# Kernel tuning notes

Hardware: AMD Instinct MI355X
Metric: run time of the kernel (lower is better)

The kernel has to match this reference:

```python
import jax, jax.numpy as jnp
import numpy as np

D_L = 64
HIDDEN = 64
CUBE = (D_L + 1) ** 3  # 274625


def setup_inputs() -> dict:
    key = jax.random.key(0)
    ks = jax.random.split(key, 9)
    B = 512
    l = jax.random.normal(ks[0], (B, D_L), dtype=jnp.float32)
    a = jax.random.normal(ks[1], (B, D_L), dtype=jnp.float32)
    v = jax.random.normal(ks[2], (B, D_L), dtype=jnp.float32)
    # Linear params (xavier-ish scale)
    W1 = jax.random.normal(ks[3], (CUBE, HIDDEN), dtype=jnp.float32) * (1.0 / np.sqrt(CUBE))
    b1 = jnp.zeros((HIDDEN,), dtype=jnp.float32)
    W2 = jax.random.normal(ks[4], (HIDDEN, HIDDEN), dtype=jnp.float32) * (1.0 / np.sqrt(HIDDEN))
    b2 = jnp.zeros((HIDDEN,), dtype=jnp.float32)
    W3 = jax.random.normal(ks[5], (HIDDEN, D_L), dtype=jnp.float32) * (1.0 / np.sqrt(HIDDEN))
    b3 = jnp.zeros((D_L,), dtype=jnp.float32)
    return {"l": l, "a": a, "v": v, "W1": W1, "b1": b1, "W2": W2, "b2": b2, "W3": W3, "b3": b3}


def reference(l, a, v, W1, b1, W2, b2, W3, b3):
    B = a.shape[0]
    ones = jnp.ones((B, 1), dtype=a.dtype)
    a_h = jnp.concatenate([ones, a], axis=1)  # [B, d+1]
    v_h = jnp.concatenate([ones, v], axis=1)
    t_h = jnp.concatenate([ones, l], axis=1)
    # fusion[b, i, j, k] = a_h[b,i] * v_h[b,j] * t_h[b,k]; flattened row-major (i,j,k)
    fusion = jnp.einsum('bi,bj,bk->bijk', a_h, v_h, t_h).reshape(B, -1)  # [B, (d+1)^3]
    h = jnp.tanh(fusion @ W1 + b1)
    h = jnp.tanh(h @ W2 + b2)
    out = jnp.tanh(h @ W3 + b3)
    return out
```

## Files before the change

### kernel.cpp

```cpp
#include <hip/hip_runtime.h>
#include <hip/hip_fp16.h>


typedef _Float16 f16;
typedef f16 f16x8 __attribute__((ext_vector_type(8)));
typedef f16 f16x2 __attribute__((ext_vector_type(2)));
typedef float f32x4 __attribute__((ext_vector_type(4)));

#define WS_AT      0
#define WS_VT      131072
#define WS_A16     262144
#define WS_V16     327680
#define WS_L16     393216
#define WS_PART    458752

__global__ __launch_bounds__(256) void prep_kernel(
    const float* __restrict__ l, const float* __restrict__ a, const float* __restrict__ v,
    float* __restrict__ aT, float* __restrict__ vT,
    f16* __restrict__ a16, f16* __restrict__ v16, f16* __restrict__ l16)
{
  int g = blockIdx.x * 256 + threadIdx.x;
  int which = g >> 15;
  int idx = g & 32767;
  switch (which) {
    case 0: aT[idx] = a[((idx & 511) << 6) + (idx >> 9)]; break;
    case 1: vT[idx] = v[((idx & 511) << 6) + (idx >> 9)]; break;
    case 2: a16[idx] = (f16)a[idx]; break;
    case 3: v16[idx] = (f16)v[idx]; break;
    case 4: l16[idx] = (f16)l[idx]; break;
  }
}

__device__ __forceinline__ void seg_decode(int s, int& ia, int& iv, int& isel,
                                           int& rowbase, int& rowstride) {
  if (s < 4096)      { int i = s >> 6, j = s & 63; ia = i; iv = j; isel = 0;
                       rowbase = (i+1)*4225 + (j+1)*65 + 1; rowstride = 1; }
  else if (s < 4160) { int i = s - 4096; ia = i; iv = -1; isel = 2;
                       rowbase = (i+1)*4225 + 65; rowstride = 65; }
  else if (s < 4224) { int i = s - 4160; ia = i; iv = -1; isel = 0;
                       rowbase = (i+1)*4225 + 1; rowstride = 1; }
  else if (s < 4288) { int j = s - 4224; ia = -1; iv = j; isel = 0;
                       rowbase = (j+1)*65 + 1; rowstride = 1; }
  else if (s == 4288){ ia = -1; iv = -1; isel = 1; rowbase = 4225; rowstride = 4225; }
  else if (s == 4289){ ia = -1; iv = -1; isel = 2; rowbase = 65;   rowstride = 65; }
  else               { ia = -1; iv = -1; isel = 0; rowbase = 1;    rowstride = 1; }
}

__global__ __launch_bounds__(512, 2) void fusion_gemm(
    const float* __restrict__ W1,
    const float* __restrict__ aT, const float* __restrict__ vT,
    const f16* __restrict__ a16, const f16* __restrict__ v16, const f16* __restrict__ l16,
    f16* __restrict__ partials)
{
  __shared__ f16 l_lds[512 * 64];
  __shared__ f16 btile[2][64 * 64];
  __shared__ f16 pl[2][512];

  const int tid  = threadIdx.x;
  const int bid  = blockIdx.x;
  const int lane = tid & 63;
  const int wave = tid >> 6;
  const int l15  = lane & 15;
  const int l4   = lane >> 4;

  #pragma unroll
  for (int it = 0; it < 8; ++it) {
    int idx = (it << 9) + tid;
    int row = idx >> 3, ch = idx & 7;
    f16x8 val = *(const f16x8*)(l16 + (idx << 3));
    *(f16x8*)&l_lds[(row << 6) + ((ch ^ (row & 7)) << 3)] = val;
  }

  const int s0   = bid * 16 + min(bid, 195);
  const int nseg = 16 + (bid < 195 ? 1 : 0);

  f32x4 acc[4][4] = {};

  const int n_st = tid & 63;
  const int g_st = tid >> 6;

  float wv[8]; float spa, spv;

  {
    int ia, iv, isel, rb, rs;
    seg_decode(s0, ia, iv, isel, rb, rs);
    const float* src = W1 + (long)(rb + g_st * 8 * rs) * 64 + n_st;
    #pragma unroll
    for (int r = 0; r < 8; ++r) wv[r] = src[(long)r * rs * 64];
    spa = (ia >= 0) ? aT[(ia << 9) + tid] : 1.0f;
    spv = (iv >= 0) ? vT[(iv << 9) + tid] : 1.0f;
  }

  for (int ss = 0; ss < nseg; ++ss) {
    const int buf = ss & 1;
    {
      f16x8 c;
      #pragma unroll
      for (int r = 0; r < 8; ++r) c[r] = (f16)wv[r];
      *(f16x8*)&btile[buf][(n_st << 6) + ((g_st ^ (n_st & 7)) << 3)] = c;
      pl[buf][tid] = (f16)(spa * spv);
    }
    if (ss + 1 < nseg) {
      int ia, iv, isel, rb, rs;
      seg_decode(s0 + ss + 1, ia, iv, isel, rb, rs);
      const float* src = W1 + (long)(rb + g_st * 8 * rs) * 64 + n_st;
      #pragma unroll
      for (int r = 0; r < 8; ++r) wv[r] = src[(long)r * rs * 64];
      spa = (ia >= 0) ? aT[(ia << 9) + tid] : 1.0f;
      spv = (iv >= 0) ? vT[(iv << 9) + tid] : 1.0f;
    }
    __syncthreads();
    {
      int ia, iv, isel, rb, rs;
      seg_decode(s0 + ss, ia, iv, isel, rb, rs);
      const f16* gptr = (isel == 1) ? a16 : v16;
      #pragma unroll
      for (int ks = 0; ks < 2; ++ks) {
        f16x8 bf[4], af[4];
        #pragma unroll
        for (int nt = 0; nt < 4; ++nt) {
          int n = (nt << 4) + l15;
          bf[nt] = *(const f16x8*)&btile[buf][(n << 6) + ((((ks << 2) + l4) ^ (n & 7)) << 3)];
        }
        #pragma unroll
        for (int mt = 0; mt < 4; ++mt) {
          int b = (wave << 6) + (mt << 4) + l15;
          f16 p = pl[buf][b];
          f16x8 lv;
          if (isel == 0) {
            lv = *(const f16x8*)&l_lds[(b << 6) + ((((ks << 2) + l4) ^ (b & 7)) << 3)];
          } else {
            lv = *(const f16x8*)(gptr + (b << 6) + (ks << 5) + (l4 << 3));
          }
          f16x2 pp = { p, p };
          f16x2* lvp = (f16x2*)&lv;
          f16x2* afp = (f16x2*)&af[mt];
          afp[0] = lvp[0] * pp; afp[1] = lvp[1] * pp;
          afp[2] = lvp[2] * pp; afp[3] = lvp[3] * pp;
        }
        #pragma unroll
        for (int mt = 0; mt < 4; ++mt)
          #pragma unroll
          for (int nt = 0; nt < 4; ++nt)
            acc[mt][nt] = __builtin_amdgcn_mfma_f32_16x16x32_f16(af[mt], bf[nt], acc[mt][nt], 0, 0, 0);
      }
    }
  }

  #pragma unroll
  for (int mt = 0; mt < 4; ++mt)
    #pragma unroll
    for (int nt = 0; nt < 4; ++nt)
      #pragma unroll
      for (int r = 0; r < 4; ++r) {
        int row = (wave << 6) + (mt << 4) + (l4 << 2) + r;
        int col = (nt << 4) + l15;
        partials[(((long)bid << 9) + row) * 64 + col] = (f16)acc[mt][nt][r];
      }
}

__global__ __launch_bounds__(256) void tail_kernel(
    const f16* __restrict__ partials, const float* __restrict__ W1, const float* __restrict__ b1,
    const float* __restrict__ W2, const float* __restrict__ b2,
    const float* __restrict__ W3, const float* __restrict__ b3, float* __restrict__ out)
{
  __shared__ float red[4][64];
  __shared__ float hbuf[64];
  __shared__ float h2buf[64];
  const int row = blockIdx.x;
  const int t = threadIdx.x;
  const int n = t & 63;
  const int q = t >> 6;

  float s_[4] = {0.f, 0.f, 0.f, 0.f};
  for (int i = 0; i < 64; i += 4) {
    #pragma unroll
    for (int u = 0; u < 4; ++u) {
      int p = ((i + u) << 2) + q;
      s_[u] += (float)partials[((((long)p << 9) + row) << 6) + n];
    }
  }
  red[q][n] = s_[0] + s_[1] + s_[2] + s_[3];
  __syncthreads();
  if (t < 64) {
    float h = red[0][n] + red[1][n] + red[2][n] + red[3][n] + b1[n] + W1[n];
    hbuf[n] = tanhf(h);
  }
  __syncthreads();
  if (t < 64) {
    float acc = b2[n];
    #pragma unroll 8
    for (int k = 0; k < 64; ++k) acc += hbuf[k] * W2[(k << 6) + n];
    h2buf[n] = tanhf(acc);
  }
  __syncthreads();
  if (t < 64) {
    float acc = b3[n];
    #pragma unroll 8
    for (int k = 0; k < 64; ++k) acc += h2buf[k] * W3[(k << 6) + n];
    out[(row << 6) + n] = tanhf(acc);
  }
}

extern "C" void kernel_launch(void* const* d_in, const int* in_sizes, int n_in,
                              void* d_out, int out_size, void* d_ws, size_t ws_size,
                              hipStream_t stream) {
  const float* l  = (const float*)d_in[0];
  const float* a  = (const float*)d_in[1];
  const float* v  = (const float*)d_in[2];
  const float* W1 = (const float*)d_in[3];
  const float* b1 = (const float*)d_in[4];
  const float* W2 = (const float*)d_in[5];
  const float* b2 = (const float*)d_in[6];
  const float* W3 = (const float*)d_in[7];
  const float* b3 = (const float*)d_in[8];
  float* out = (float*)d_out;

  char* ws = (char*)d_ws;
  float* aT  = (float*)(ws + WS_AT);
  float* vT  = (float*)(ws + WS_VT);
  f16*   a16 = (f16*)(ws + WS_A16);
  f16*   v16 = (f16*)(ws + WS_V16);
  f16*   l16 = (f16*)(ws + WS_L16);
  f16*   partials = (f16*)(ws + WS_PART);

  hipLaunchKernelGGL(prep_kernel, dim3(640), dim3(256), 0, stream,
                     l, a, v, aT, vT, a16, v16, l16);
  hipLaunchKernelGGL(fusion_gemm, dim3(256), dim3(512), 0, stream,
                     W1, aT, vT, a16, v16, l16, partials);
  hipLaunchKernelGGL(tail_kernel, dim3(512), dim3(256), 0, stream,
                     partials, W1, b1, W2, b2, W3, b3, out);
}
```

Measured before the change: 63.01 us.

## Restructure fusion GEMM to 1024-thread blocks with register-resident l fragments

The fusion GEMM now launches 1024 threads per block, with two half-blocks each staging one W1 segment so two segments are processed per barrier. Blocks take a fixed 18 segments each, and out-of-range segments are zeroed through a new decode sentinel. The l operand moves from a 64KB LDS copy into per-wave registers, and each wave covers 32 rows instead of 64, which cuts LDS use and raises occupancy. The partials layout is transposed to row-major per batch row so the tail kernel can do contiguous vectorized reads; the tradeoff is more threads per block and higher register pressure.

```diff
diff --git a/kernel.cpp b/kernel.cpp
--- a/kernel.cpp
+++ b/kernel.cpp
@@ -43,18 +43,18 @@
                        rowbase = (j+1)*65 + 1; rowstride = 1; }
   else if (s == 4288){ ia = -1; iv = -1; isel = 1; rowbase = 4225; rowstride = 4225; }
   else if (s == 4289){ ia = -1; iv = -1; isel = 2; rowbase = 65;   rowstride = 65; }
-  else               { ia = -1; iv = -1; isel = 0; rowbase = 1;    rowstride = 1; }
-}
-
-__global__ __launch_bounds__(512, 2) void fusion_gemm(
+  else if (s == 4290){ ia = -1; iv = -1; isel = 0; rowbase = 1;    rowstride = 1; }
+  else               { ia = -2; iv = -1; isel = 0; rowbase = 1;    rowstride = 1; }
+}
+
+__global__ __launch_bounds__(1024, 4) void fusion_gemm(
     const float* __restrict__ W1,
     const float* __restrict__ aT, const float* __restrict__ vT,
     const f16* __restrict__ a16, const f16* __restrict__ v16, const f16* __restrict__ l16,
     f16* __restrict__ partials)
 {
-  __shared__ f16 l_lds[512 * 64];
-  __shared__ f16 btile[2][64 * 64];
-  __shared__ f16 pl[2][512];
+  __shared__ f16 btile[4][64 * 64];
+  __shared__ f16 pl[4][512];
 
   const int tid  = threadIdx.x;
   const int bid  = blockIdx.x;
@@ -62,100 +62,106 @@
   const int wave = tid >> 6;
   const int l15  = lane & 15;
   const int l4   = lane >> 4;
-
-  #pragma unroll
-  for (int it = 0; it < 8; ++it) {
-    int idx = (it << 9) + tid;
-    int row = idx >> 3, ch = idx & 7;
-    f16x8 val = *(const f16x8*)(l16 + (idx << 3));
-    *(f16x8*)&l_lds[(row << 6) + ((ch ^ (row & 7)) << 3)] = val;
-  }
-
-  const int s0   = bid * 16 + min(bid, 195);
-  const int nseg = 16 + (bid < 195 ? 1 : 0);
-
-  f32x4 acc[4][4] = {};
-
-  const int n_st = tid & 63;
-  const int g_st = tid >> 6;
-
-  float wv[8]; float spa, spv;
-
-  {
-    int ia, iv, isel, rb, rs;
-    seg_decode(s0, ia, iv, isel, rb, rs);
-    const float* src = W1 + (long)(rb + g_st * 8 * rs) * 64 + n_st;
-    #pragma unroll
-    for (int r = 0; r < 8; ++r) wv[r] = src[(long)r * rs * 64];
-    spa = (ia >= 0) ? aT[(ia << 9) + tid] : 1.0f;
-    spv = (iv >= 0) ? vT[(iv << 9) + tid] : 1.0f;
-  }
-
-  for (int ss = 0; ss < nseg; ++ss) {
-    const int buf = ss & 1;
+  const int h    = tid >> 9;
+  const int t9   = tid & 511;
+  const int n_st = t9 & 63;
+  const int g_st = t9 >> 6;
+
+  f16x8 lfrag[2][2];
+  #pragma unroll
+  for (int mt = 0; mt < 2; ++mt) {
+    int row = (wave << 5) + (mt << 4) + l15;
+    #pragma unroll
+    for (int ks = 0; ks < 2; ++ks)
+      lfrag[mt][ks] = *(const f16x8*)(l16 + (row << 6) + (ks << 5) + (l4 << 3));
+  }
+
+  f32x4 acc[2][4] = {};
+
+  float wv[2][8];
+  float sp[2][2];
+
+#define ISSUE_LOADS(SET, SEG) do {                                              \
+    int ia_, iv_, isel_, rb_, rs_; seg_decode((SEG), ia_, iv_, isel_, rb_, rs_);\
+    const int rs64_ = rs_ << 6;                                                 \
+    const float* src_ = W1 + (size_t)rb_ * 64 + (size_t)(g_st << 3) * rs64_ + n_st; \
+    _Pragma("unroll")                                                           \
+    for (int r_ = 0; r_ < 8; ++r_) wv[SET][r_] = src_[(size_t)r_ * rs64_];      \
+    sp[SET][0] = (ia_ >= 0) ? aT[(ia_ << 9) + t9] : (ia_ == -1 ? 1.0f : 0.0f);  \
+    sp[SET][1] = (iv_ >= 0) ? vT[(iv_ << 9) + t9] : 1.0f;                       \
+  } while (0)
+
+  ISSUE_LOADS(0, bid * 18 + h);
+
+  #pragma unroll
+  for (int pp = 0; pp < 9; ++pp) {
+    const int cur = pp & 1;
+    const int sbw = (cur << 1) + h;
     {
       f16x8 c;
-      #pragma unroll
-      for (int r = 0; r < 8; ++r) c[r] = (f16)wv[r];
-      *(f16x8*)&btile[buf][(n_st << 6) + ((g_st ^ (n_st & 7)) << 3)] = c;
-      pl[buf][tid] = (f16)(spa * spv);
+      if (cur == 0) {
+        #pragma unroll
+        for (int r = 0; r < 8; ++r) c[r] = (f16)wv[0][r];
+      } else {
+        #pragma unroll
+        for (int r = 0; r < 8; ++r) c[r] = (f16)wv[1][r];
+      }
+      *(f16x8*)&btile[sbw][(n_st << 6) + ((g_st ^ (n_st & 7)) << 3)] = c;
+      pl[sbw][t9] = (f16)(sp[cur][0] * sp[cur][1]);
     }
-    if (ss + 1 < nseg) {
-      int ia, iv, isel, rb, rs;
-      seg_decode(s0 + ss + 1, ia, iv, isel, rb, rs);
-      const float* src = W1 + (long)(rb + g_st * 8 * rs) * 64 + n_st;
-      #pragma unroll
-      for (int r = 0; r < 8; ++r) wv[r] = src[(long)r * rs * 64];
-      spa = (ia >= 0) ? aT[(ia << 9) + tid] : 1.0f;
-      spv = (iv >= 0) ? vT[(iv << 9) + tid] : 1.0f;
+    if (pp < 8) {
+      if (cur == 0) ISSUE_LOADS(1, bid * 18 + (pp + 1) * 2 + h);
+      else          ISSUE_LOADS(0, bid * 18 + (pp + 1) * 2 + h);
     }
-    __syncthreads();
-    {
-      int ia, iv, isel, rb, rs;
-      seg_decode(s0 + ss, ia, iv, isel, rb, rs);
-      const f16* gptr = (isel == 1) ? a16 : v16;
+    asm volatile("s_waitcnt lgkmcnt(0)\n\ts_barrier" ::: "memory");
+    __builtin_amdgcn_sched_barrier(0);
+
+    #pragma unroll
+    for (int sidx = 0; sidx < 2; ++sidx) {
+      const int sb = (cur << 1) + sidx;
+      int s = bid * 18 + pp * 2 + sidx;
+      int ia_, iv_, isel, rb_, rs_;
+      seg_decode(s, ia_, iv_, isel, rb_, rs_);
+      const f16* gsrc = (isel == 1) ? a16 : v16;
       #pragma unroll
       for (int ks = 0; ks < 2; ++ks) {
-        f16x8 bf[4], af[4];
+        f16x8 bf[4];
         #pragma unroll
         for (int nt = 0; nt < 4; ++nt) {
           int n = (nt << 4) + l15;
-          bf[nt] = *(const f16x8*)&btile[buf][(n << 6) + ((((ks << 2) + l4) ^ (n & 7)) << 3)];
+          bf[nt] = *(const f16x8*)&btile[sb][(n << 6) + ((((ks << 2) + l4) ^ (n & 7)) << 3)];
         }
         #pragma unroll
-        for (int mt = 0; mt < 4; ++mt) {
-          int b = (wave << 6) + (mt << 4) + l15;
-          f16 p = pl[buf][b];
+        for (int mt = 0; mt < 2; ++mt) {
+          int row = (wave << 5) + (mt << 4) + l15;
+          f16 ps = pl[sb][row];
           f16x8 lv;
-          if (isel == 0) {
-            lv = *(const f16x8*)&l_lds[(b << 6) + ((((ks << 2) + l4) ^ (b & 7)) << 3)];
-          } else {
-            lv = *(const f16x8*)(gptr + (b << 6) + (ks << 5) + (l4 << 3));
-          }
-          f16x2 pp = { p, p };
+          if (isel == 0) lv = lfrag[mt][ks];
+          else           lv = *(const f16x8*)(gsrc + (row << 6) + (ks << 5) + (l4 << 3));
+          f16x2 ps2 = { ps, ps };
+          f16x8 av;
           f16x2* lvp = (f16x2*)&lv;
-          f16x2* afp = (f16x2*)&af[mt];
-          afp[0] = lvp[0] * pp; afp[1] = lvp[1] * pp;
-          afp[2] = lvp[2] * pp; afp[3] = lvp[3] * pp;
-        }
-        #pragma unroll
-        for (int mt = 0; mt < 4; ++mt)
+          f16x2* avp = (f16x2*)&av;
+          avp[0] = lvp[0] * ps2; avp[1] = lvp[1] * ps2;
+          avp[2] = lvp[2] * ps2; avp[3] = lvp[3] * ps2;
           #pragma unroll
           for (int nt = 0; nt < 4; ++nt)
-            acc[mt][nt] = __builtin_amdgcn_mfma_f32_16x16x32_f16(af[mt], bf[nt], acc[mt][nt], 0, 0, 0);
+            acc[mt][nt] = __builtin_amdgcn_mfma_f32_16x16x32_f16(av, bf[nt], acc[mt][nt], 0, 0, 0);
+        }
       }
     }
   }
-
-  #pragma unroll
-  for (int mt = 0; mt < 4; ++mt)
+#undef ISSUE_LOADS
+
+  #pragma unroll
+  for (int mt = 0; mt < 2; ++mt)
     #pragma unroll
     for (int nt = 0; nt < 4; ++nt)
       #pragma unroll
       for (int r = 0; r < 4; ++r) {
-        int row = (wave << 6) + (mt << 4) + (l4 << 2) + r;
+        int row = (wave << 5) + (mt << 4) + (l4 << 2) + r;
         int col = (nt << 4) + l15;
-        partials[(((long)bid << 9) + row) * 64 + col] = (f16)acc[mt][nt][r];
+        partials[((size_t)row << 14) + (bid << 6) + col] = (f16)acc[mt][nt][r];
       }
 }
 
@@ -164,41 +170,42 @@
     const float* __restrict__ W2, const float* __restrict__ b2,
     const float* __restrict__ W3, const float* __restrict__ b3, float* __restrict__ out)
 {
-  __shared__ float red[4][64];
+  __shared__ float red[256][8];
   __shared__ float hbuf[64];
   __shared__ float h2buf[64];
   const int row = blockIdx.x;
   const int t = threadIdx.x;
-  const int n = t & 63;
-  const int q = t >> 6;
-
-  float s_[4] = {0.f, 0.f, 0.f, 0.f};
-  for (int i = 0; i < 64; i += 4) {
-    #pragma unroll
-    for (int u = 0; u < 4; ++u) {
-      int p = ((i + u) << 2) + q;
-      s_[u] += (float)partials[((((long)p << 9) + row) << 6) + n];
-    }
-  }
-  red[q][n] = s_[0] + s_[1] + s_[2] + s_[3];
+  const f16* base = partials + ((size_t)row << 14);
+
+  float s[8] = {0.f,0.f,0.f,0.f,0.f,0.f,0.f,0.f};
+  #pragma unroll
+  for (int j = 0; j < 8; ++j) {
+    f16x8 v = *(const f16x8*)(base + (((j << 8) + t) << 3));
+    #pragma unroll
+    for (int e = 0; e < 8; ++e) s[e] += (float)v[e];
+  }
+  #pragma unroll
+  for (int e = 0; e < 8; ++e) red[t][e] = s[e];
   __syncthreads();
   if (t < 64) {
-    float h = red[0][n] + red[1][n] + red[2][n] + red[3][n] + b1[n] + W1[n];
-    hbuf[n] = tanhf(h);
+    float acc = b1[t] + W1[t];
+    #pragma unroll
+    for (int k = 0; k < 32; ++k) acc += red[(t >> 3) + (k << 3)][t & 7];
+    hbuf[t] = tanhf(acc);
   }
   __syncthreads();
   if (t < 64) {
-    float acc = b2[n];
+    float acc = b2[t];
     #pragma unroll 8
-    for (int k = 0; k < 64; ++k) acc += hbuf[k] * W2[(k << 6) + n];
-    h2buf[n] = tanhf(acc);
+    for (int k = 0; k < 64; ++k) acc += hbuf[k] * W2[(k << 6) + t];
+    h2buf[t] = tanhf(acc);
   }
   __syncthreads();
   if (t < 64) {
-    float acc = b3[n];
+    float acc = b3[t];
     #pragma unroll 8
-    for (int k = 0; k < 64; ++k) acc += h2buf[k] * W3[(k << 6) + n];
-    out[(row << 6) + n] = tanhf(acc);
+    for (int k = 0; k < 64; ++k) acc += h2buf[k] * W3[(k << 6) + t];
+    out[(row << 6) + t] = tanhf(acc);
   }
 }
 
@@ -226,7 +233,7 @@
 
   hipLaunchKernelGGL(prep_kernel, dim3(640), dim3(256), 0, stream,
                      l, a, v, aT, vT, a16, v16, l16);
-  hipLaunchKernelGGL(fusion_gemm, dim3(256), dim3(512), 0, stream,
+  hipLaunchKernelGGL(fusion_gemm, dim3(256), dim3(1024), 0, stream,
                      W1, aT, vT, a16, v16, l16, partials);
   hipLaunchKernelGGL(tail_kernel, dim3(512), dim3(256), 0, stream,
                      partials, W1, b1, W2, b2, W3, b3, out);
```

New measurement: 63.04 us. About the same (+0.0%).
